# Kernel optimization log

Measured on AMD Instinct MI355X. Metric: run time of the kernel, lower is better.

## Reference

```python
import jax, jax.numpy as jnp
import numpy as np


def _reverse_padded(x, lengths):
    # x: [T, B, D]; reverse each sequence within its own length (packed-seq semantics)
    T = x.shape[0]
    t = jnp.arange(T)[:, None]                                   # [T, 1]
    idx = jnp.where(t < lengths[None, :], lengths[None, :] - 1 - t, t)  # [T, B]
    return jnp.take_along_axis(x, idx[:, :, None], axis=0)


def _lstm_dir(x, w_ih, w_hh, b):
    # single-direction LSTM, torch gate order (i, f, g, o). x: [T, B, Din]
    T, B, _ = x.shape
    H = w_hh.shape[1]
    xg = jnp.einsum('tbi,gi->tbg', x, w_ih) + b  # precompute input projections [T,B,4H]

    def step(carry, g_x):
        h, c = carry
        g = g_x + h @ w_hh.T
        i, f, gc, o = jnp.split(g, 4, axis=-1)
        c = jax.nn.sigmoid(f) * c + jax.nn.sigmoid(i) * jnp.tanh(gc)
        h = jax.nn.sigmoid(o) * jnp.tanh(c)
        return (h, c), h

    h0 = jnp.zeros((B, H), x.dtype)
    _, hs = jax.lax.scan(step, (h0, h0), xg)
    return hs  # [T, B, H]


def _bilstm_layer(x, lengths, wf, whf, bf, wr, whr, br):
    fwd = _lstm_dir(x, wf, whf, bf)
    rev = _reverse_padded(_lstm_dir(_reverse_padded(x, lengths), wr, whr, br), lengths)
    return jnp.concatenate([fwd, rev], axis=-1)  # [T, B, 2H]


def setup_inputs() -> dict:
    T, B, D, H = 256, 128, 300, 256
    key = jax.random.key(0)
    ks = jax.random.split(key, 24)
    stdv = 1.0 / np.sqrt(H)

    def u(k, shape):
        return jax.random.uniform(k, shape, jnp.float32, -stdv, stdv)

    inp = {
        'x': jax.random.normal(ks[0], (T, B, D), jnp.float32),
        'lengths': jax.random.randint(ks[1], (B,), 1, T + 1),
        # layer 0 forward / reverse
        'w_ih_l0': u(ks[2], (4 * H, D)), 'w_hh_l0': u(ks[3], (4 * H, H)),
        'b_ih_l0': u(ks[4], (4 * H,)), 'b_hh_l0': u(ks[5], (4 * H,)),
        'w_ih_l0r': u(ks[6], (4 * H, D)), 'w_hh_l0r': u(ks[7], (4 * H, H)),
        'b_ih_l0r': u(ks[8], (4 * H,)), 'b_hh_l0r': u(ks[9], (4 * H,)),
        # layer 1 forward / reverse (input dim 2H)
        'w_ih_l1': u(ks[10], (4 * H, 2 * H)), 'w_hh_l1': u(ks[11], (4 * H, H)),
        'b_ih_l1': u(ks[12], (4 * H,)), 'b_hh_l1': u(ks[13], (4 * H,)),
        'w_ih_l1r': u(ks[14], (4 * H, 2 * H)), 'w_hh_l1r': u(ks[15], (4 * H, H)),
        'b_ih_l1r': u(ks[16], (4 * H,)), 'b_hh_l1r': u(ks[17], (4 * H,)),
        # attention MLP + context vector
        'mlp_w': u(ks[18], (2 * H, 2 * H)),
        'mlp_b': u(ks[19], (2 * H,)),
        'ctx': jax.random.normal(ks[20], (2 * H,), jnp.float32) * 0.1,
    }
    return inp


def reference(x, lengths, w_ih_l0, w_hh_l0, b_ih_l0, b_hh_l0,
              w_ih_l0r, w_hh_l0r, b_ih_l0r, b_hh_l0r,
              w_ih_l1, w_hh_l1, b_ih_l1, b_hh_l1,
              w_ih_l1r, w_hh_l1r, b_ih_l1r, b_hh_l1r,
              mlp_w, mlp_b, ctx):
    lengths = jnp.maximum(lengths, 1)
    h1 = _bilstm_layer(x, lengths, w_ih_l0, w_hh_l0, b_ih_l0 + b_hh_l0,
                       w_ih_l0r, w_hh_l0r, b_ih_l0r + b_hh_l0r)
    h2 = _bilstm_layer(h1, lengths, w_ih_l1, w_hh_l1, b_ih_l1 + b_hh_l1,
                       w_ih_l1r, w_hh_l1r, b_ih_l1r + b_hh_l1r)
    out = h2.transpose(1, 0, 2)                                  # [B, T, 2H]
    ann = jnp.tanh(jnp.einsum('btd,ed->bte', out, mlp_w) + mlp_b)  # [B, T, 2H]
    scores = ann @ ctx                                           # [B, T]
    T = out.shape[1]
    mask = jnp.arange(T)[None, :] < lengths[:, None]             # [B, T]
    w = jax.nn.softmax(jnp.where(mask, scores, -1e9), axis=1)    # masked softmax over time
    return jnp.einsum('bt,btd->bd', w, out)                      # [B, 2H]
```

## Files before the change

### kernel.cpp

```cpp
#include <hip/hip_runtime.h>


#define T_ 256
#define B_ 128
#define D_ 300
#define H_ 256
#define G4H 1024
#define H2 512
#define LDK 40
#define LDA 264
#define XGS 76
#define RSLOTS 4

typedef __attribute__((ext_vector_type(8))) short bf16x8;
typedef __attribute__((ext_vector_type(4))) short short4v;
typedef __attribute__((ext_vector_type(4))) float f32x4;

#define MFMA16(a, b, c) __builtin_amdgcn_mfma_f32_16x16x32_bf16(a, b, c, 0, 0, 0)
#define ATOM_ST(p, v) __hip_atomic_store((p), (v), __ATOMIC_RELAXED, __HIP_MEMORY_SCOPE_AGENT)
#define ATOM_LD(p) __hip_atomic_load((p), __ATOMIC_RELAXED, __HIP_MEMORY_SCOPE_AGENT)

__device__ __forceinline__ float sigf(float x) { return 1.f / (1.f + __expf(-x)); }
__device__ __forceinline__ float tanhfast(float x) { return 2.f / (1.f + __expf(-2.f * x)) - 1.f; }

__device__ __forceinline__ short hi_bf16(float x) {
  return (short)(__float_as_uint(x) >> 16);
}
__device__ __forceinline__ short lo_bf16(float x) {
  float lo = x - __uint_as_float(__float_as_uint(x) & 0xFFFF0000u);
  return (short)(__float_as_uint(lo) >> 16);
}

__device__ __forceinline__ void split_f4(const float4 v, short* hp, short* lp) {
  short4v h, l;
  h.x = hi_bf16(v.x); l.x = lo_bf16(v.x);
  h.y = hi_bf16(v.y); l.y = lo_bf16(v.y);
  h.z = hi_bf16(v.z); l.z = lo_bf16(v.z);
  h.w = hi_bf16(v.w); l.w = lo_bf16(v.w);
  *(short4v*)hp = h;
  *(short4v*)lp = l;
}

__device__ __forceinline__ void split8(const float4 v0, const float4 v1,
                                       bf16x8* hp, bf16x8* lp) {
  bf16x8 h, l;
  h[0] = hi_bf16(v0.x); l[0] = lo_bf16(v0.x);
  h[1] = hi_bf16(v0.y); l[1] = lo_bf16(v0.y);
  h[2] = hi_bf16(v0.z); l[2] = lo_bf16(v0.z);
  h[3] = hi_bf16(v0.w); l[3] = lo_bf16(v0.w);
  h[4] = hi_bf16(v1.x); l[4] = lo_bf16(v1.x);
  h[5] = hi_bf16(v1.y); l[5] = lo_bf16(v1.y);
  h[6] = hi_bf16(v1.z); l[6] = lo_bf16(v1.z);
  h[7] = hi_bf16(v1.w); l[7] = lo_bf16(v1.w);
  *hp = h; *lp = l;
}

__global__ __launch_bounds__(256, 2) void proj_gemm2(
    const float* __restrict__ X,
    const float* __restrict__ W0, const float* __restrict__ W1,
    const float* __restrict__ b1f, const float* __restrict__ b2f,
    const float* __restrict__ b1r, const float* __restrict__ b2r,
// ... 136 lines not shown
      split_f4(wv, &Wh[ro], &Wl[ro]);
    }
    __syncthreads();

    bf16x8 ah[4], al[4], bh[4], bl[4];
#pragma unroll
    for (int mt = 0; mt < 4; mt++) {
      const int ro = (mb + mt * 16 + r16) * LDK + quad * 8;
      ah[mt] = *(const bf16x8*)&Xh[ro];
      al[mt] = *(const bf16x8*)&Xl[ro];
    }
#pragma unroll
    for (int nt = 0; nt < 4; nt++) {
      const int ro = (nb + nt * 16 + r16) * LDK + quad * 8;
      bh[nt] = *(const bf16x8*)&Wh[ro];
      bl[nt] = *(const bf16x8*)&Wl[ro];
    }
#pragma unroll
    for (int mt = 0; mt < 4; mt++)
#pragma unroll
      for (int nt = 0; nt < 4; nt++) {
        acc[mt][nt] = __builtin_amdgcn_mfma_f32_16x16x32_bf16(ah[mt], bh[nt], acc[mt][nt], 0, 0, 0);
        acc[mt][nt] = __builtin_amdgcn_mfma_f32_16x16x32_bf16(ah[mt], bl[nt], acc[mt][nt], 0, 0, 0);
        acc[mt][nt] = __builtin_amdgcn_mfma_f32_16x16x32_bf16(al[mt], bh[nt], acc[mt][nt], 0, 0, 0);
      }
    __syncthreads();
  }

  float bb4[4], cc4[4];
#pragma unroll
  for (int nt = 0; nt < 4; nt++) {
    const int col = n0 + nb + nt * 16 + r16;
    bb4[nt] = mlp_b[col];
    cc4[nt] = ctx[col];
  }
#pragma unroll
  for (int mt = 0; mt < 4; mt++) {
#pragma unroll
    for (int reg = 0; reg < 4; reg++) {
      float ssum = 0.f;
#pragma unroll
      for (int nt = 0; nt < 4; nt++)
        ssum += tanhfast(acc[mt][nt][reg] + bb4[nt]) * cc4[nt];
      ssum += __shfl_xor(ssum, 1);
      ssum += __shfl_xor(ssum, 2);
      ssum += __shfl_xor(ssum, 4);
      ssum += __shfl_xor(ssum, 8);
      if (r16 == 0)
        atomicAdd(&scores[m0 + mb + mt * 16 + quad * 4 + reg], ssum);
    }
  }
}

__global__ __launch_bounds__(256, 1) void lstm_fused(
    float* __restrict__ xgF, float* __restrict__ xgR,
    const float* __restrict__ XSRC,
    const float* __restrict__ whF, const float* __restrict__ whR,
    const float* __restrict__ wihF, const float* __restrict__ wihR,
    const float* __restrict__ b1f, const float* __restrict__ b2f,
    const float* __restrict__ b1r, const float* __restrict__ b2r,
    const int* __restrict__ lengths, float* __restrict__ hout,
    float* __restrict__ ring, int K)
{
  __shared__ short Ah[16 * LDA], Al[16 * LDA];
  __shared__ float gbuf[8 * 128];
  __shared__ short PXh[128 * LDK], PXl[128 * LDK];
  __shared__ short PWh[128 * LDK], PWl[128 * LDK];

  const int tid = threadIdx.x;
  const int blk = blockIdx.x;
  const int s = blk >> 5;
  const int d = (blk >> 4) & 1;
  const int g = blk & 15;
  float* __restrict__ xgd = d ? xgR : xgF;
  const float* __restrict__ wh = d ? whR : whF;
  const float* __restrict__ wih = d ? wihR : wihF;
  const float* __restrict__ bias1 = d ? b1r : b1f;
  const float* __restrict__ bias2 = d ? b2r : b2f;
  unsigned* __restrict__ ring32 = (unsigned*)ring;

  const int lane = tid & 63;
  const int w = tid >> 6;
  const int r16 = lane & 15, quad = lane >> 4;

  const int cb = tid >> 5;
  const int hl = tid & 31;
  const int b = g * 8 + cb;
  const int hdim = s * 32 + hl;
  const int k0 = hl * 8;

  const int sr = tid >> 3;
  const int sc = (tid & 7) * 4;
  const int mb = (w & 1) * 64, nb = (w >> 1) * 64;
  const int n0 = s * 128;
  const int KITERS = (K + 31) >> 5;

  bf16x8 bh[2][8], bl[2][8];
#pragma unroll
  for (int nt = 0; nt < 2; nt++)
#pragma unroll
    for (int kt = 0; kt < 8; kt++) {
      const float* wr = wh + (size_t)(w * 256 + s * 32 + nt * 16 + r16) * 256
                           + kt * 32 + quad * 8;
      float4 v0 = *(const float4*)(wr);
      float4 v1 = *(const float4*)(wr + 4);
      split8(v0, v1, &bh[nt][kt], &bl[nt][kt]);
    }

  f32x4 pacc[4][4];
#pragma unroll
  for (int i = 0; i < 4; i++)
#pragma unroll
    for (int j = 0; j < 4; j++) pacc[i][j] = (f32x4){0.f, 0.f, 0.f, 0.f};

  {
    int* za = (int*)Ah;
    int* zb = (int*)Al;
    for (int i = tid; i < (16 * LDA) / 2; i += 256) { za[i] = 0; zb[i] = 0; }
  }
  float c = 0.f;
  int lb = lengths[b]; if (lb < 1) lb = 1;
  const float* xr0 = xgd + (size_t)b * 1024 + hdim;
  float x0 = ATOM_LD(xr0), x1 = ATOM_LD(xr0 + 256);
  float x2 = ATOM_LD(xr0 + 512), x3 = ATOM_LD(xr0 + 768);
  __syncthreads();

  for (int t = 0; t < T_; t++) {
    const bool last = (t == T_ - 1);

    f32x4 aH0 = {0.f,0.f,0.f,0.f}, aM0 = {0.f,0.f,0.f,0.f}, aL0 = {0.f,0.f,0.f,0.f};
    f32x4 aH1 = {0.f,0.f,0.f,0.f}, aM1 = {0.f,0.f,0.f,0.f}, aL1 = {0.f,0.f,0.f,0.f};
#pragma unroll
    for (int kt = 0; kt < 8; kt++) {
      const int ro = r16 * LDA + kt * 32 + quad * 8;
      bf16x8 ahf = *(const bf16x8*)&Ah[ro];
      bf16x8 alf = *(const bf16x8*)&Al[ro];
      aH0 = MFMA16(ahf, bh[0][kt], aH0);
      aM0 = MFMA16(ahf, bl[0][kt], aM0);
      aL0 = MFMA16(alf, bh[0][kt], aL0);
      aH1 = MFMA16(ahf, bh[1][kt], aH1);
      aM1 = MFMA16(ahf, bl[1][kt], aM1);
      aL1 = MFMA16(alf, bh[1][kt], aL1);
    }
    if (quad < 2) {
#pragma unroll
      for (int reg = 0; reg < 4; reg++) {
        gbuf[(quad * 4 + reg) * 128 + w * 32 + r16]      = aH0[reg] + aM0[reg] + aL0[reg];
        gbuf[(quad * 4 + reg) * 128 + w * 32 + 16 + r16] = aH1[reg] + aM1[reg] + aL1[reg];
      }
    }
    __syncthreads();

    const float gi = gbuf[cb * 128 +       hl] + x0;
    const float gf = gbuf[cb * 128 +  32 + hl] + x1;
    const float gg = gbuf[cb * 128 +  64 + hl] + x2;
    const float go = gbuf[cb * 128 +  96 + hl] + x3;
    const float si = sigf(gi), sf = sigf(gf);
    const float tg = tanhfast(gg), so = sigf(go);
    c = sf * c + si * tg;
    const float h = so * tanhfast(c);
    if (!last) {
      const unsigned hu = (unsigned)(unsigned short)hi_bf16(h);
      const unsigned lu = (unsigned)(unsigned short)lo_bf16(h);
      const unsigned pv = (hu << 16) | (lu & 0xFFFEu) | (unsigned)((t >> 2) & 1);
      ATOM_ST(&ring32[(((t & 3) * 2 + d) * 128 + b) * 256 + hdim], pv);
    }
    const int tin = d ? ((t < lb) ? (lb - 1 - t) : t) : t;
    hout[((size_t)tin * 128 + b) * 512 + d * 256 + hdim] = h;

    if (t < 192) {
      const int wj = t >> 4, ki = t & 15;
      const int y = 64 + wj * 16 + g;
      if (ki < KITERS) {
        const int gk = ki * 32 + sc;
        const bool kin = (gk < K);
#pragma unroll
        for (int p = 0; p < 4; p++) {
          const int r = sr + p * 32;
          float4 xv = {0.f, 0.f, 0.f, 0.f}, wv = {0.f, 0.f, 0.f, 0.f};
          if (kin) {
            int ss = y;
            if (d) {
              int lbr = lengths[r]; if (lbr < 1) lbr = 1;
              ss = (y < lbr) ? (lbr - 1 - y) : y;
            }
            xv = *(const float4*)(XSRC + ((size_t)ss * 128 + r) * K + gk);
            wv = *(const float4*)(wih + (size_t)(n0 + r) * K + gk);
          }
          const int ro = (sr + p * 32) * LDK + sc;
          split_f4(xv, &PXh[ro], &PXl[ro]);
          split_f4(wv, &PWh[ro], &PWl[ro]);
        }
        __syncthreads();

        bf16x8 pah[4], pal[4], pbh[4], pbl[4];
#pragma unroll
        for (int mt = 0; mt < 4; mt++) {
          const int ro = (mb + mt * 16 + r16) * LDK + quad * 8;
          pah[mt] = *(const bf16x8*)&PXh[ro];
          pal[mt] = *(const bf16x8*)&PXl[ro];
        }
#pragma unroll
        for (int nt = 0; nt < 4; nt++) {
          const int ro = (nb + nt * 16 + r16) * LDK + quad * 8;
          pbh[nt] = *(const bf16x8*)&PWh[ro];
          pbl[nt] = *(const bf16x8*)&PWl[ro];
        }
#pragma unroll
        for (int mt = 0; mt < 4; mt++)
#pragma unroll
          for (int nt = 0; nt < 4; nt++) {
            pacc[mt][nt] = MFMA16(pah[mt], pbh[nt], pacc[mt][nt]);
            pacc[mt][nt] = MFMA16(pah[mt], pbl[nt], pacc[mt][nt]);
            pacc[mt][nt] = MFMA16(pal[mt], pbh[nt], pacc[mt][nt]);
          }
      }
      if (ki == 15) {
        const int yslot = y % XGS;
        float bsum[4];
#pragma unroll
        for (int nt = 0; nt < 4; nt++) {
          const int col = n0 + nb + nt * 16 + r16;
          bsum[nt] = bias1[col] + bias2[col];
        }
#pragma unroll
        for (int mt = 0; mt < 4; mt++) {
          const int row = mb + mt * 16 + quad * 4;
#pragma unroll
          for (int nt = 0; nt < 4; nt++) {
            const int col = n0 + nb + nt * 16 + r16;
            float* Cp = xgd + ((size_t)yslot * 128 + row) * 1024 + col;
#pragma unroll
            for (int reg = 0; reg < 4; reg++)
              ATOM_ST(&Cp[(size_t)reg * 1024], pacc[mt][nt][reg] + bsum[nt]);
            pacc[mt][nt] = (f32x4){0.f, 0.f, 0.f, 0.f};
          }
        }
      }
    }

    if (!last) {
      const int ns = (t + 1) % XGS;
      const float* xn = xgd + ((size_t)ns * 128 + b) * 1024 + hdim;
      const float nx0 = ATOM_LD(xn), nx1 = ATOM_LD(xn + 256);
      const float nx2 = ATOM_LD(xn + 512), nx3 = ATOM_LD(xn + 768);

      const unsigned* ru = ring32 + (((t & 3) * 2 + d) * 128 + g * 8 + cb) * 256 + k0;
      const unsigned par = (unsigned)((t >> 2) & 1);
      unsigned uv[8];
      int it = 0;
      for (;;) {
        bool ok = true;
#pragma unroll
        for (int j = 0; j < 8; j++) {
          uv[j] = ATOM_LD(&ru[j]);
          ok &= ((uv[j] & 1u) == par);
        }
        if (ok || ++it >= 100000) break;
      }
      bf16x8 hv, lv;
#pragma unroll
      for (int j = 0; j < 8; j++) {
        hv[j] = (short)(uv[j] >> 16);
        lv[j] = (short)(uv[j] & 0xFFFFu);
      }
      *(bf16x8*)&Ah[cb * LDA + k0] = hv;
      *(bf16x8*)&Al[cb * LDA + k0] = lv;

      x0 = nx0; x1 = nx1; x2 = nx2; x3 = nx3;
      __syncthreads();
    }
  }
}

__global__ __launch_bounds__(256) void attn_final(
    const float* __restrict__ h2, const float* __restrict__ scores,
    const int* __restrict__ lengths, float* __restrict__ out)
{
  __shared__ float sl[256];
  __shared__ float red[256];
  const int b = blockIdx.x, tid = threadIdx.x;
  int lb = lengths[b]; if (lb < 1) lb = 1;
  const float sc = scores[(size_t)tid * 128 + b];
  const bool valid = (tid < lb);
  red[tid] = valid ? sc : -1e30f;
  __syncthreads();
  for (int off = 128; off > 0; off >>= 1) {
    if (tid < off) red[tid] = fmaxf(red[tid], red[tid + off]);
    __syncthreads();
  }
  const float mx = red[0];
  __syncthreads();
  const float p = valid ? __expf(sc - mx) : 0.f;
  red[tid] = p;
  __syncthreads();
  for (int off = 128; off > 0; off >>= 1) {
    if (tid < off) red[tid] += red[tid + off];
    __syncthreads();
  }
  const float inv = 1.f / red[0];
  __syncthreads();
  sl[tid] = p * inv;
  __syncthreads();

  float ax = 0.f, ay = 0.f;
  const int dd = tid * 2;
  for (int t = 0; t < 256; t++) {
    const float w = sl[t];
    if (w != 0.f) {
      const float* row = h2 + ((size_t)t * 128 + b) * 512 + dd;
      ax += w * row[0];
      ay += w * row[1];
    }
  }
  float2 r; r.x = ax; r.y = ay;
  *(float2*)(out + (size_t)b * 512 + dd) = r;
}

extern "C" void kernel_launch(void* const* d_in, const int* in_sizes, int n_in,
                              void* d_out, int out_size, void* d_ws, size_t ws_size,
                              hipStream_t stream) {
  (void)in_sizes; (void)n_in; (void)out_size; (void)ws_size;
  const float* x        = (const float*)d_in[0];
  const int*   lengths  = (const int*)d_in[1];
  const float* w_ih_l0  = (const float*)d_in[2];
  const float* w_hh_l0  = (const float*)d_in[3];
  const float* b_ih_l0  = (const float*)d_in[4];
  const float* b_hh_l0  = (const float*)d_in[5];
  const float* w_ih_l0r = (const float*)d_in[6];
  const float* w_hh_l0r = (const float*)d_in[7];
  const float* b_ih_l0r = (const float*)d_in[8];
  const float* b_hh_l0r = (const float*)d_in[9];
  const float* w_ih_l1  = (const float*)d_in[10];
  const float* w_hh_l1  = (const float*)d_in[11];
  const float* b_ih_l1  = (const float*)d_in[12];
  const float* b_hh_l1  = (const float*)d_in[13];
  const float* w_ih_l1r = (const float*)d_in[14];
  const float* w_hh_l1r = (const float*)d_in[15];
  const float* b_ih_l1r = (const float*)d_in[16];
  const float* b_hh_l1r = (const float*)d_in[17];
  const float* mlp_w    = (const float*)d_in[18];
  const float* mlp_b    = (const float*)d_in[19];
  const float* ctx      = (const float*)d_in[20];
  float* out = (float*)d_out;

  float* ws = (float*)d_ws;
  const size_t XG76  = (size_t)XGS * B_ * G4H;
  const size_t H_SZ  = (size_t)T_ * B_ * H2;
  const size_t RINGF = (size_t)RSLOTS * 2 * B_ * H_;
  float* xgF    = ws;
  float* xgR    = xgF + XG76;
  float* h1     = xgR + XG76;
  float* h2     = h1 + H_SZ;
  float* ring   = h2 + H_SZ;
  float* scores = ring + RINGF;

  (void)hipMemsetAsync(scores, 0, 32768 * 4, stream);

  dim3 blk(256);
  const dim3 pgrid(G4H / 128, 64, 2);

  proj_gemm2<<<pgrid, blk, 0, stream>>>(x, w_ih_l0, w_ih_l0r,
                                        b_ih_l0, b_hh_l0, b_ih_l0r, b_hh_l0r,
                                        xgF, xgR, G4H, D_, lengths, 0);
  (void)hipMemsetAsync(ring, 0xFF, RINGF * 4, stream);
  lstm_fused<<<256, blk, 0, stream>>>(xgF, xgR, x, w_hh_l0, w_hh_l0r,
                                      w_ih_l0, w_ih_l0r,
                                      b_ih_l0, b_hh_l0, b_ih_l0r, b_hh_l0r,
                                      lengths, h1, ring, D_);
  proj_gemm2<<<pgrid, blk, 0, stream>>>(h1, w_ih_l1, w_ih_l1r,
                                        b_ih_l1, b_hh_l1, b_ih_l1r, b_hh_l1r,
                                        xgF, xgR, G4H, H2, lengths, 0);
  (void)hipMemsetAsync(ring, 0xFF, RINGF * 4, stream);
  lstm_fused<<<256, blk, 0, stream>>>(xgF, xgR, h1, w_hh_l1, w_hh_l1r,
                                      w_ih_l1, w_ih_l1r,
                                      b_ih_l1, b_hh_l1, b_ih_l1r, b_hh_l1r,
                                      lengths, h2, ring, H2);
  attn_gemm<<<dim3(H2 / 128, (T_ * B_) / 128), blk, 0, stream>>>(h2, mlp_w, mlp_b, ctx, scores, T_ * B_, H2, H2);
  attn_final<<<B_, blk, 0, stream>>>(h2, scores, lengths, out);
}
```

Before: 2.639 ms.

## Warp-specialize LSTM kernel: separate recurrence and projection waves with register prefetch

```diff
diff --git a/kernel.cpp b/kernel.cpp
--- a/kernel.cpp
+++ b/kernel.cpp
@@ -249,7 +249,7 @@
   }
 }
 
-__global__ __launch_bounds__(256, 1) void lstm_fused(
+__global__ __launch_bounds__(512, 2) void lstm_fused(
     float* __restrict__ xgF, float* __restrict__ xgR,
     const float* __restrict__ XSRC,
     const float* __restrict__ whF, const float* __restrict__ whR,
@@ -269,204 +269,247 @@
   const int s = blk >> 5;
   const int d = (blk >> 4) & 1;
   const int g = blk & 15;
+  const bool is_lstm = (tid < 256);
   float* __restrict__ xgd = d ? xgR : xgF;
   const float* __restrict__ wh = d ? whR : whF;
   const float* __restrict__ wih = d ? wihR : wihF;
   const float* __restrict__ bias1 = d ? b1r : b1f;
   const float* __restrict__ bias2 = d ? b2r : b2f;
   unsigned* __restrict__ ring32 = (unsigned*)ring;
-
+  const int KITERS = (K + 31) >> 5;
+
+  const int w = tid >> 6;
   const int lane = tid & 63;
-  const int w = tid >> 6;
   const int r16 = lane & 15, quad = lane >> 4;
-
-  const int cb = tid >> 5;
+  const int cb = (tid >> 5) & 7;
   const int hl = tid & 31;
   const int b = g * 8 + cb;
   const int hdim = s * 32 + hl;
   const int k0 = hl * 8;
 
-  const int sr = tid >> 3;
-  const int sc = (tid & 7) * 4;
-  const int mb = (w & 1) * 64, nb = (w >> 1) * 64;
+  const int pt = tid & 255;
+  const int sr = pt >> 3;
+  const int sc = (pt & 7) * 4;
+  const int w2 = pt >> 6;
+  const int pmb = (w2 & 1) * 64, pnb = (w2 >> 1) * 64;
+  const int pr16 = (pt & 63) & 15, pquad = (pt & 63) >> 4;
   const int n0 = s * 128;
-  const int KITERS = (K + 31) >> 5;
-
-  bf16x8 bh[2][8], bl[2][8];
-#pragma unroll
-  for (int nt = 0; nt < 2; nt++)
-#pragma unroll
-    for (int kt = 0; kt < 8; kt++) {
-      const float* wr = wh + (size_t)(w * 256 + s * 32 + nt * 16 + r16) * 256
-                           + kt * 32 + quad * 8;
-      float4 v0 = *(const float4*)(wr);
-      float4 v1 = *(const float4*)(wr + 4);
-      split8(v0, v1, &bh[nt][kt], &bl[nt][kt]);
-    }
-
-  f32x4 pacc[4][4];
-#pragma unroll
-  for (int i = 0; i < 4; i++)
-#pragma unroll
-    for (int j = 0; j < 4; j++) pacc[i][j] = (f32x4){0.f, 0.f, 0.f, 0.f};
 
   {
     int* za = (int*)Ah;
     int* zb = (int*)Al;
-    for (int i = tid; i < (16 * LDA) / 2; i += 256) { za[i] = 0; zb[i] = 0; }
-  }
+    for (int i = tid; i < (16 * LDA) / 2; i += 512) { za[i] = 0; zb[i] = 0; }
+  }
+
+  bf16x8 bh[2][8], bl[2][8];
   float c = 0.f;
-  int lb = lengths[b]; if (lb < 1) lb = 1;
-  const float* xr0 = xgd + (size_t)b * 1024 + hdim;
-  float x0 = ATOM_LD(xr0), x1 = ATOM_LD(xr0 + 256);
-  float x2 = ATOM_LD(xr0 + 512), x3 = ATOM_LD(xr0 + 768);
+  int lb = 1;
+  float x0 = 0.f, x1 = 0.f, x2 = 0.f, x3 = 0.f;
+  int lenp[4];
+  float4 pfX[4], pfW[4];
+  f32x4 pacc[4][4];
+
+  if (is_lstm) {
+#pragma unroll
+    for (int nt = 0; nt < 2; nt++)
+#pragma unroll
+      for (int kt = 0; kt < 8; kt++) {
+        const float* wr = wh + (size_t)(w * 256 + s * 32 + nt * 16 + r16) * 256
+                             + kt * 32 + quad * 8;
+        float4 v0 = *(const float4*)(wr);
+        float4 v1 = *(const float4*)(wr + 4);
+        split8(v0, v1, &bh[nt][kt], &bl[nt][kt]);
+      }
+    lb = lengths[b]; if (lb < 1) lb = 1;
+    const float* xr0 = xgd + (size_t)b * 1024 + hdim;
+    x0 = ATOM_LD(xr0); x1 = ATOM_LD(xr0 + 256);
+    x2 = ATOM_LD(xr0 + 512); x3 = ATOM_LD(xr0 + 768);
+  } else {
+#pragma unroll
+    for (int p = 0; p < 4; p++) {
+      int lv = lengths[sr + p * 32]; if (lv < 1) lv = 1;
+      lenp[p] = lv;
+    }
+#pragma unroll
+    for (int i = 0; i < 4; i++)
+#pragma unroll
+      for (int j = 0; j < 4; j++) pacc[i][j] = (f32x4){0.f, 0.f, 0.f, 0.f};
+    {
+      const int y = 64 + g;
+      const int gk = sc;
+#pragma unroll
+      for (int p = 0; p < 4; p++) {
+        const int r = sr + p * 32;
+        int ss = y;
+        if (d) ss = (y < lenp[p]) ? (lenp[p] - 1 - y) : y;
+        pfX[p] = *(const float4*)(XSRC + ((size_t)ss * 128 + r) * K + gk);
+        pfW[p] = *(const float4*)(wih + (size_t)(n0 + r) * K + gk);
+      }
+    }
+  }
   __syncthreads();
 
   for (int t = 0; t < T_; t++) {
     const bool last = (t == T_ - 1);
 
-    f32x4 aH0 = {0.f,0.f,0.f,0.f}, aM0 = {0.f,0.f,0.f,0.f}, aL0 = {0.f,0.f,0.f,0.f};
-    f32x4 aH1 = {0.f,0.f,0.f,0.f}, aM1 = {0.f,0.f,0.f,0.f}, aL1 = {0.f,0.f,0.f,0.f};
-#pragma unroll
-    for (int kt = 0; kt < 8; kt++) {
-      const int ro = r16 * LDA + kt * 32 + quad * 8;
-      bf16x8 ahf = *(const bf16x8*)&Ah[ro];
-      bf16x8 alf = *(const bf16x8*)&Al[ro];
-      aH0 = MFMA16(ahf, bh[0][kt], aH0);
-      aM0 = MFMA16(ahf, bl[0][kt], aM0);
-      aL0 = MFMA16(alf, bh[0][kt], aL0);
-      aH1 = MFMA16(ahf, bh[1][kt], aH1);
-      aM1 = MFMA16(ahf, bl[1][kt], aM1);
-      aL1 = MFMA16(alf, bh[1][kt], aL1);
-    }
-    if (quad < 2) {
-#pragma unroll
-      for (int reg = 0; reg < 4; reg++) {
-        gbuf[(quad * 4 + reg) * 128 + w * 32 + r16]      = aH0[reg] + aM0[reg] + aL0[reg];
-        gbuf[(quad * 4 + reg) * 128 + w * 32 + 16 + r16] = aH1[reg] + aM1[reg] + aL1[reg];
-      }
-    }
-    __syncthreads();
-
-    const float gi = gbuf[cb * 128 +       hl] + x0;
-    const float gf = gbuf[cb * 128 +  32 + hl] + x1;
-    const float gg = gbuf[cb * 128 +  64 + hl] + x2;
-    const float go = gbuf[cb * 128 +  96 + hl] + x3;
-    const float si = sigf(gi), sf = sigf(gf);
-    const float tg = tanhfast(gg), so = sigf(go);
-    c = sf * c + si * tg;
-    const float h = so * tanhfast(c);
-    if (!last) {
-      const unsigned hu = (unsigned)(unsigned short)hi_bf16(h);
-      const unsigned lu = (unsigned)(unsigned short)lo_bf16(h);
-      const unsigned pv = (hu << 16) | (lu & 0xFFFEu) | (unsigned)((t >> 2) & 1);
-      ATOM_ST(&ring32[(((t & 3) * 2 + d) * 128 + b) * 256 + hdim], pv);
-    }
-    const int tin = d ? ((t < lb) ? (lb - 1 - t) : t) : t;
-    hout[((size_t)tin * 128 + b) * 512 + d * 256 + hdim] = h;
-
-    if (t < 192) {
-      const int wj = t >> 4, ki = t & 15;
-      const int y = 64 + wj * 16 + g;
-      if (ki < KITERS) {
-        const int gk = ki * 32 + sc;
-        const bool kin = (gk < K);
-#pragma unroll
-        for (int p = 0; p < 4; p++) {
-          const int r = sr + p * 32;
-          float4 xv = {0.f, 0.f, 0.f, 0.f}, wv = {0.f, 0.f, 0.f, 0.f};
-          if (kin) {
-            int ss = y;
-            if (d) {
-              int lbr = lengths[r]; if (lbr < 1) lbr = 1;
-              ss = (y < lbr) ? (lbr - 1 - y) : y;
-            }
-            xv = *(const float4*)(XSRC + ((size_t)ss * 128 + r) * K + gk);
-            wv = *(const float4*)(wih + (size_t)(n0 + r) * K + gk);
-          }
-          const int ro = (sr + p * 32) * LDK + sc;
-          split_f4(xv, &PXh[ro], &PXl[ro]);
-          split_f4(wv, &PWh[ro], &PWl[ro]);
+    if (is_lstm) {
+      f32x4 aH0 = {0.f,0.f,0.f,0.f}, aM0 = {0.f,0.f,0.f,0.f}, aL0 = {0.f,0.f,0.f,0.f};
+      f32x4 aH1 = {0.f,0.f,0.f,0.f}, aM1 = {0.f,0.f,0.f,0.f}, aL1 = {0.f,0.f,0.f,0.f};
+#pragma unroll
+      for (int kt = 0; kt < 8; kt++) {
+        const int ro = r16 * LDA + kt * 32 + quad * 8;
+        bf16x8 ahf = *(const bf16x8*)&Ah[ro];
+        bf16x8 alf = *(const bf16x8*)&Al[ro];
+        aH0 = MFMA16(ahf, bh[0][kt], aH0);
+        aM0 = MFMA16(ahf, bl[0][kt], aM0);
+        aL0 = MFMA16(alf, bh[0][kt], aL0);
+        aH1 = MFMA16(ahf, bh[1][kt], aH1);
+        aM1 = MFMA16(ahf, bl[1][kt], aM1);
+        aL1 = MFMA16(alf, bh[1][kt], aL1);
+      }
+      if (quad < 2) {
+#pragma unroll
+        for (int reg = 0; reg < 4; reg++) {
+          gbuf[(quad * 4 + reg) * 128 + w * 32 + r16]      = aH0[reg] + aM0[reg] + aL0[reg];
+          gbuf[(quad * 4 + reg) * 128 + w * 32 + 16 + r16] = aH1[reg] + aM1[reg] + aL1[reg];
         }
-        __syncthreads();
-
-        bf16x8 pah[4], pal[4], pbh[4], pbl[4];
-#pragma unroll
-        for (int mt = 0; mt < 4; mt++) {
-          const int ro = (mb + mt * 16 + r16) * LDK + quad * 8;
-          pah[mt] = *(const bf16x8*)&PXh[ro];
-          pal[mt] = *(const bf16x8*)&PXl[ro];
-        }
-#pragma unroll
-        for (int nt = 0; nt < 4; nt++) {
-          const int ro = (nb + nt * 16 + r16) * LDK + quad * 8;
-          pbh[nt] = *(const bf16x8*)&PWh[ro];
-          pbl[nt] = *(const bf16x8*)&PWl[ro];
-        }
-#pragma unroll
-        for (int mt = 0; mt < 4; mt++)
-#pragma unroll
-          for (int nt = 0; nt < 4; nt++) {
-            pacc[mt][nt] = MFMA16(pah[mt], pbh[nt], pacc[mt][nt]);
-            pacc[mt][nt] = MFMA16(pah[mt], pbl[nt], pacc[mt][nt]);
-            pacc[mt][nt] = MFMA16(pal[mt], pbh[nt], pacc[mt][nt]);
-          }
-      }
-      if (ki == 15) {
-        const int yslot = y % XGS;
-        float bsum[4];
-#pragma unroll
-        for (int nt = 0; nt < 4; nt++) {
-          const int col = n0 + nb + nt * 16 + r16;
-          bsum[nt] = bias1[col] + bias2[col];
-        }
-#pragma unroll
-        for (int mt = 0; mt < 4; mt++) {
-          const int row = mb + mt * 16 + quad * 4;
-#pragma unroll
-          for (int nt = 0; nt < 4; nt++) {
-            const int col = n0 + nb + nt * 16 + r16;
-            float* Cp = xgd + ((size_t)yslot * 128 + row) * 1024 + col;
-#pragma unroll
-            for (int reg = 0; reg < 4; reg++)
-              ATOM_ST(&Cp[(size_t)reg * 1024], pacc[mt][nt][reg] + bsum[nt]);
-            pacc[mt][nt] = (f32x4){0.f, 0.f, 0.f, 0.f};
+      }
+    } else {
+      if (t < 192) {
+        const int ki = t & 15;
+        if (ki < KITERS) {
+#pragma unroll
+          for (int p = 0; p < 4; p++) {
+            const int gk = ki * 32 + sc;
+            const int ro = (sr + p * 32) * LDK + sc;
+            float4 xv = {0.f,0.f,0.f,0.f}, wv = {0.f,0.f,0.f,0.f};
+            if (gk < K) { xv = pfX[p]; wv = pfW[p]; }
+            split_f4(xv, &PXh[ro], &PXl[ro]);
+            split_f4(wv, &PWh[ro], &PWl[ro]);
           }
         }
       }
     }
-
-    if (!last) {
-      const int ns = (t + 1) % XGS;
-      const float* xn = xgd + ((size_t)ns * 128 + b) * 1024 + hdim;
-      const float nx0 = ATOM_LD(xn), nx1 = ATOM_LD(xn + 256);
-      const float nx2 = ATOM_LD(xn + 512), nx3 = ATOM_LD(xn + 768);
-
-      const unsigned* ru = ring32 + (((t & 3) * 2 + d) * 128 + g * 8 + cb) * 256 + k0;
-      const unsigned par = (unsigned)((t >> 2) & 1);
-      unsigned uv[8];
-      int it = 0;
-      for (;;) {
-        bool ok = true;
+    __syncthreads();
+
+    if (is_lstm) {
+      const float gi = gbuf[cb * 128 +       hl] + x0;
+      const float gf = gbuf[cb * 128 +  32 + hl] + x1;
+      const float gg = gbuf[cb * 128 +  64 + hl] + x2;
+      const float go = gbuf[cb * 128 +  96 + hl] + x3;
+      const float si = sigf(gi), sf = sigf(gf);
+      const float tg = tanhfast(gg), so = sigf(go);
+      c = sf * c + si * tg;
+      const float h = so * tanhfast(c);
+      if (!last) {
+        const unsigned hu = (unsigned)(unsigned short)hi_bf16(h);
+        const unsigned lu = (unsigned)(unsigned short)lo_bf16(h);
+        const unsigned pv = (hu << 16) | (lu & 0xFFFEu) | (unsigned)((t >> 2) & 1);
+        ATOM_ST(&ring32[(((t & 3) * 2 + d) * 128 + b) * 256 + hdim], pv);
+      }
+      const int tin = d ? ((t < lb) ? (lb - 1 - t) : t) : t;
+      hout[((size_t)tin * 128 + b) * 512 + d * 256 + hdim] = h;
+
+      if (!last) {
+        const int ns = (t + 1) % XGS;
+        const float* xn = xgd + ((size_t)ns * 128 + b) * 1024 + hdim;
+        const float nx0 = ATOM_LD(xn), nx1 = ATOM_LD(xn + 256);
+        const float nx2 = ATOM_LD(xn + 512), nx3 = ATOM_LD(xn + 768);
+
+        const unsigned* ru = ring32 + (((t & 3) * 2 + d) * 128 + g * 8 + cb) * 256 + k0;
+        const unsigned par = (unsigned)((t >> 2) & 1);
+        unsigned uv[8];
+        int it = 0;
+        for (;;) {
+          bool ok = true;
+#pragma unroll
+          for (int j = 0; j < 8; j++) {
+            uv[j] = ATOM_LD(&ru[j]);
+            ok &= ((uv[j] & 1u) == par);
+          }
+          if (ok || ++it >= 100000) break;
+        }
+        bf16x8 hv, lv;
 #pragma unroll
         for (int j = 0; j < 8; j++) {
-          uv[j] = ATOM_LD(&ru[j]);
-          ok &= ((uv[j] & 1u) == par);
+          hv[j] = (short)(uv[j] >> 16);
+          lv[j] = (short)(uv[j] & 0xFFFFu);
         }
-        if (ok || ++it >= 100000) break;
-      }
-      bf16x8 hv, lv;
-#pragma unroll
-      for (int j = 0; j < 8; j++) {
-        hv[j] = (short)(uv[j] >> 16);
-        lv[j] = (short)(uv[j] & 0xFFFFu);
-      }
-      *(bf16x8*)&Ah[cb * LDA + k0] = hv;
-      *(bf16x8*)&Al[cb * LDA + k0] = lv;
-
-      x0 = nx0; x1 = nx1; x2 = nx2; x3 = nx3;
-      __syncthreads();
-    }
+        *(bf16x8*)&Ah[cb * LDA + k0] = hv;
+        *(bf16x8*)&Al[cb * LDA + k0] = lv;
+
+        x0 = nx0; x1 = nx1; x2 = nx2; x3 = nx3;
+      }
+    } else {
+      if (t < 192) {
+        const int ki = t & 15;
+        if (ki < KITERS) {
+          bf16x8 pah[4], pal[4], pbh[4], pbl[4];
+#pragma unroll
+          for (int mt = 0; mt < 4; mt++) {
+            const int ro = (pmb + mt * 16 + pr16) * LDK + pquad * 8;
+            pah[mt] = *(const bf16x8*)&PXh[ro];
+            pal[mt] = *(const bf16x8*)&PXl[ro];
+          }
+#pragma unroll
+          for (int nt = 0; nt < 4; nt++) {
+            const int ro = (pnb + nt * 16 + pr16) * LDK + pquad * 8;
+            pbh[nt] = *(const bf16x8*)&PWh[ro];
+            pbl[nt] = *(const bf16x8*)&PWl[ro];
+          }
+#pragma unroll
+          for (int mt = 0; mt < 4; mt++)
+#pragma unroll
+            for (int nt = 0; nt < 4; nt++) {
+              pacc[mt][nt] = MFMA16(pah[mt], pbh[nt], pacc[mt][nt]);
+              pacc[mt][nt] = MFMA16(pah[mt], pbl[nt], pacc[mt][nt]);
+              pacc[mt][nt] = MFMA16(pal[mt], pbh[nt], pacc[mt][nt]);
+            }
+        }
+        if (ki == 15) {
+          const int y = 64 + (t >> 4) * 16 + g;
+          const int yslot = y % XGS;
+          float bsum[4];
+#pragma unroll
+          for (int nt = 0; nt < 4; nt++) {
+            const int col = n0 + pnb + nt * 16 + pr16;
+            bsum[nt] = bias1[col] + bias2[col];
+          }
+#pragma unroll
+          for (int mt = 0; mt < 4; mt++) {
+            const int row = pmb + mt * 16 + pquad * 4;
+#pragma unroll
+            for (int nt = 0; nt < 4; nt++) {
+              const int col = n0 + pnb + nt * 16 + pr16;
+              float* Cp = xgd + ((size_t)yslot * 128 + row) * 1024 + col;
+#pragma unroll
+              for (int reg = 0; reg < 4; reg++)
+                ATOM_ST(&Cp[(size_t)reg * 1024], pacc[mt][nt][reg] + bsum[nt]);
+              pacc[mt][nt] = (f32x4){0.f, 0.f, 0.f, 0.f};
+            }
+          }
+        }
+      }
+      const int tn = t + 1;
+      if (tn < 192) {
+        const int kin = tn & 15;
+        if (kin < KITERS) {
+          const int y = 64 + (tn >> 4) * 16 + g;
+          const int gk = kin * 32 + sc;
+          if (gk < K) {
+#pragma unroll
+            for (int p = 0; p < 4; p++) {
+              const int r = sr + p * 32;
+              int ss = y;
+              if (d) ss = (y < lenp[p]) ? (lenp[p] - 1 - y) : y;
+              pfX[p] = *(const float4*)(XSRC + ((size_t)ss * 128 + r) * K + gk);
+              pfW[p] = *(const float4*)(wih + (size_t)(n0 + r) * K + gk);
+            }
+          }
+        }
+      }
+    }
+    __syncthreads();
   }
 }
 
@@ -561,18 +604,18 @@
                                         b_ih_l0, b_hh_l0, b_ih_l0r, b_hh_l0r,
                                         xgF, xgR, G4H, D_, lengths, 0);
   (void)hipMemsetAsync(ring, 0xFF, RINGF * 4, stream);
-  lstm_fused<<<256, blk, 0, stream>>>(xgF, xgR, x, w_hh_l0, w_hh_l0r,
-                                      w_ih_l0, w_ih_l0r,
-                                      b_ih_l0, b_hh_l0, b_ih_l0r, b_hh_l0r,
-                                      lengths, h1, ring, D_);
+  lstm_fused<<<256, dim3(512), 0, stream>>>(xgF, xgR, x, w_hh_l0, w_hh_l0r,
+                                            w_ih_l0, w_ih_l0r,
+                                            b_ih_l0, b_hh_l0, b_ih_l0r, b_hh_l0r,
+                                            lengths, h1, ring, D_);
   proj_gemm2<<<pgrid, blk, 0, stream>>>(h1, w_ih_l1, w_ih_l1r,
                                         b_ih_l1, b_hh_l1, b_ih_l1r, b_hh_l1r,
                                         xgF, xgR, G4H, H2, lengths, 0);
   (void)hipMemsetAsync(ring, 0xFF, RINGF * 4, stream);
-  lstm_fused<<<256, blk, 0, stream>>>(xgF, xgR, h1, w_hh_l1, w_hh_l1r,
-                                      w_ih_l1, w_ih_l1r,
-                                      b_ih_l1, b_hh_l1, b_ih_l1r, b_hh_l1r,
-                                      lengths, h2, ring, H2);
+  lstm_fused<<<256, dim3(512), 0, stream>>>(xgF, xgR, h1, w_hh_l1, w_hh_l1r,
+                                            w_ih_l1, w_ih_l1r,
+                                            b_ih_l1, b_hh_l1, b_ih_l1r, b_hh_l1r,
+                                            lengths, h2, ring, H2);
   attn_gemm<<<dim3(H2 / 128, (T_ * B_) / 128), blk, 0, stream>>>(h2, mlp_w, mlp_b, ctx, scores, T_ * B_, H2, H2);
   attn_final<<<B_, blk, 0, stream>>>(h2, scores, lengths, out);
 }
```

Result: slower. 3.782 ms (+43.3%).

## Split LSTM recurrence into time chunks with separate projection blocks

Applied to the files above, without the earlier changes.

```diff
diff --git a/kernel.cpp b/kernel.cpp
--- a/kernel.cpp
+++ b/kernel.cpp
@@ -7,6 +7,7 @@
 #define H_ 256
 #define G4H 1024
 #define H2 512
+#define TC 64
 #define LDK 40
 #define LDA 264
 #define XGS 76
@@ -249,7 +250,7 @@
   }
 }
 
-__global__ __launch_bounds__(256, 1) void lstm_fused(
+__global__ __launch_bounds__(256, 2) void lstm_fused(
     float* __restrict__ xgF, float* __restrict__ xgR,
     const float* __restrict__ XSRC,
     const float* __restrict__ whF, const float* __restrict__ whR,
@@ -257,193 +258,64 @@
     const float* __restrict__ b1f, const float* __restrict__ b2f,
     const float* __restrict__ b1r, const float* __restrict__ b2r,
     const int* __restrict__ lengths, float* __restrict__ hout,
-    float* __restrict__ ring, int K)
+    float* __restrict__ ring, float* __restrict__ cbuf,
+    int* __restrict__ prog, int t0, int K, int do_proj)
 {
   __shared__ short Ah[16 * LDA], Al[16 * LDA];
   __shared__ float gbuf[8 * 128];
   __shared__ short PXh[128 * LDK], PXl[128 * LDK];
   __shared__ short PWh[128 * LDK], PWl[128 * LDK];
+  __shared__ int gflag;
 
   const int tid = threadIdx.x;
-  const int blk = blockIdx.x;
-  const int s = blk >> 5;
-  const int d = (blk >> 4) & 1;
-  const int g = blk & 15;
-  float* __restrict__ xgd = d ? xgR : xgF;
-  const float* __restrict__ wh = d ? whR : whF;
-  const float* __restrict__ wih = d ? wihR : wihF;
-  const float* __restrict__ bias1 = d ? b1r : b1f;
-  const float* __restrict__ bias2 = d ? b2r : b2f;
   unsigned* __restrict__ ring32 = (unsigned*)ring;
 
-  const int lane = tid & 63;
-  const int w = tid >> 6;
-  const int r16 = lane & 15, quad = lane >> 4;
-
-  const int cb = tid >> 5;
-  const int hl = tid & 31;
-  const int b = g * 8 + cb;
-  const int hdim = s * 32 + hl;
-  const int k0 = hl * 8;
-
-  const int sr = tid >> 3;
-  const int sc = (tid & 7) * 4;
-  const int mb = (w & 1) * 64, nb = (w >> 1) * 64;
-  const int n0 = s * 128;
-  const int KITERS = (K + 31) >> 5;
-
-  bf16x8 bh[2][8], bl[2][8];
-#pragma unroll
-  for (int nt = 0; nt < 2; nt++)
-#pragma unroll
-    for (int kt = 0; kt < 8; kt++) {
-      const float* wr = wh + (size_t)(w * 256 + s * 32 + nt * 16 + r16) * 256
-                           + kt * 32 + quad * 8;
-      float4 v0 = *(const float4*)(wr);
-      float4 v1 = *(const float4*)(wr + 4);
-      split8(v0, v1, &bh[nt][kt], &bl[nt][kt]);
-    }
-
-  f32x4 pacc[4][4];
-#pragma unroll
-  for (int i = 0; i < 4; i++)
-#pragma unroll
-    for (int j = 0; j < 4; j++) pacc[i][j] = (f32x4){0.f, 0.f, 0.f, 0.f};
-
-  {
-    int* za = (int*)Ah;
-    int* zb = (int*)Al;
-    for (int i = tid; i < (16 * LDA) / 2; i += 256) { za[i] = 0; zb[i] = 0; }
-  }
-  float c = 0.f;
-  int lb = lengths[b]; if (lb < 1) lb = 1;
-  const float* xr0 = xgd + (size_t)b * 1024 + hdim;
-  float x0 = ATOM_LD(xr0), x1 = ATOM_LD(xr0 + 256);
-  float x2 = ATOM_LD(xr0 + 512), x3 = ATOM_LD(xr0 + 768);
-  __syncthreads();
-
-  for (int t = 0; t < T_; t++) {
-    const bool last = (t == T_ - 1);
-
-    f32x4 aH0 = {0.f,0.f,0.f,0.f}, aM0 = {0.f,0.f,0.f,0.f}, aL0 = {0.f,0.f,0.f,0.f};
-    f32x4 aH1 = {0.f,0.f,0.f,0.f}, aM1 = {0.f,0.f,0.f,0.f}, aL1 = {0.f,0.f,0.f,0.f};
-#pragma unroll
-    for (int kt = 0; kt < 8; kt++) {
-      const int ro = r16 * LDA + kt * 32 + quad * 8;
-      bf16x8 ahf = *(const bf16x8*)&Ah[ro];
-      bf16x8 alf = *(const bf16x8*)&Al[ro];
-      aH0 = MFMA16(ahf, bh[0][kt], aH0);
-      aM0 = MFMA16(ahf, bl[0][kt], aM0);
-      aL0 = MFMA16(alf, bh[0][kt], aL0);
-      aH1 = MFMA16(ahf, bh[1][kt], aH1);
-      aM1 = MFMA16(ahf, bl[1][kt], aM1);
-      aL1 = MFMA16(alf, bh[1][kt], aL1);
-    }
-    if (quad < 2) {
-#pragma unroll
-      for (int reg = 0; reg < 4; reg++) {
-        gbuf[(quad * 4 + reg) * 128 + w * 32 + r16]      = aH0[reg] + aM0[reg] + aL0[reg];
-        gbuf[(quad * 4 + reg) * 128 + w * 32 + 16 + r16] = aH1[reg] + aM1[reg] + aL1[reg];
-      }
-    }
-    __syncthreads();
-
-    const float gi = gbuf[cb * 128 +       hl] + x0;
-    const float gf = gbuf[cb * 128 +  32 + hl] + x1;
-    const float gg = gbuf[cb * 128 +  64 + hl] + x2;
-    const float go = gbuf[cb * 128 +  96 + hl] + x3;
-    const float si = sigf(gi), sf = sigf(gf);
-    const float tg = tanhfast(gg), so = sigf(go);
-    c = sf * c + si * tg;
-    const float h = so * tanhfast(c);
-    if (!last) {
-      const unsigned hu = (unsigned)(unsigned short)hi_bf16(h);
-      const unsigned lu = (unsigned)(unsigned short)lo_bf16(h);
-      const unsigned pv = (hu << 16) | (lu & 0xFFFEu) | (unsigned)((t >> 2) & 1);
-      ATOM_ST(&ring32[(((t & 3) * 2 + d) * 128 + b) * 256 + hdim], pv);
-    }
-    const int tin = d ? ((t < lb) ? (lb - 1 - t) : t) : t;
-    hout[((size_t)tin * 128 + b) * 512 + d * 256 + hdim] = h;
-
-    if (t < 192) {
-      const int wj = t >> 4, ki = t & 15;
-      const int y = 64 + wj * 16 + g;
-      if (ki < KITERS) {
-        const int gk = ki * 32 + sc;
-        const bool kin = (gk < K);
-#pragma unroll
-        for (int p = 0; p < 4; p++) {
-          const int r = sr + p * 32;
-          float4 xv = {0.f, 0.f, 0.f, 0.f}, wv = {0.f, 0.f, 0.f, 0.f};
-          if (kin) {
-            int ss = y;
-            if (d) {
-              int lbr = lengths[r]; if (lbr < 1) lbr = 1;
-              ss = (y < lbr) ? (lbr - 1 - y) : y;
-            }
-            xv = *(const float4*)(XSRC + ((size_t)ss * 128 + r) * K + gk);
-            wv = *(const float4*)(wih + (size_t)(n0 + r) * K + gk);
-          }
-          const int ro = (sr + p * 32) * LDK + sc;
-          split_f4(xv, &PXh[ro], &PXl[ro]);
-          split_f4(wv, &PWh[ro], &PWl[ro]);
-        }
-        __syncthreads();
-
-        bf16x8 pah[4], pal[4], pbh[4], pbl[4];
-#pragma unroll
-        for (int mt = 0; mt < 4; mt++) {
-          const int ro = (mb + mt * 16 + r16) * LDK + quad * 8;
-          pah[mt] = *(const bf16x8*)&PXh[ro];
-          pal[mt] = *(const bf16x8*)&PXl[ro];
-        }
-#pragma unroll
-        for (int nt = 0; nt < 4; nt++) {
-          const int ro = (nb + nt * 16 + r16) * LDK + quad * 8;
-          pbh[nt] = *(const bf16x8*)&PWh[ro];
-          pbl[nt] = *(const bf16x8*)&PWl[ro];
-        }
-#pragma unroll
-        for (int mt = 0; mt < 4; mt++)
-#pragma unroll
-          for (int nt = 0; nt < 4; nt++) {
-            pacc[mt][nt] = MFMA16(pah[mt], pbh[nt], pacc[mt][nt]);
-            pacc[mt][nt] = MFMA16(pah[mt], pbl[nt], pacc[mt][nt]);
-            pacc[mt][nt] = MFMA16(pal[mt], pbh[nt], pacc[mt][nt]);
-          }
-      }
-      if (ki == 15) {
-        const int yslot = y % XGS;
-        float bsum[4];
-#pragma unroll
-        for (int nt = 0; nt < 4; nt++) {
-          const int col = n0 + nb + nt * 16 + r16;
-          bsum[nt] = bias1[col] + bias2[col];
-        }
-#pragma unroll
-        for (int mt = 0; mt < 4; mt++) {
-          const int row = mb + mt * 16 + quad * 4;
-#pragma unroll
-          for (int nt = 0; nt < 4; nt++) {
-            const int col = n0 + nb + nt * 16 + r16;
-            float* Cp = xgd + ((size_t)yslot * 128 + row) * 1024 + col;
-#pragma unroll
-            for (int reg = 0; reg < 4; reg++)
-              ATOM_ST(&Cp[(size_t)reg * 1024], pacc[mt][nt][reg] + bsum[nt]);
-            pacc[mt][nt] = (f32x4){0.f, 0.f, 0.f, 0.f};
-          }
-        }
-      }
-    }
-
-    if (!last) {
-      const int ns = (t + 1) % XGS;
-      const float* xn = xgd + ((size_t)ns * 128 + b) * 1024 + hdim;
-      const float nx0 = ATOM_LD(xn), nx1 = ATOM_LD(xn + 256);
-      const float nx2 = ATOM_LD(xn + 512), nx3 = ATOM_LD(xn + 768);
-
-      const unsigned* ru = ring32 + (((t & 3) * 2 + d) * 128 + g * 8 + cb) * 256 + k0;
-      const unsigned par = (unsigned)((t >> 2) & 1);
+  if (blockIdx.x < 256) {
+    const int blk = blockIdx.x;
+    const int s = blk >> 5;
+    const int d = (blk >> 4) & 1;
+    const int g = blk & 15;
+    float* __restrict__ xgd = d ? xgR : xgF;
+    const float* __restrict__ wh = d ? whR : whF;
+
+    const int lane = tid & 63;
+    const int w = tid >> 6;
+    const int r16 = lane & 15, quad = lane >> 4;
+    const int cb = tid >> 5;
+    const int hl = tid & 31;
+    const int b = g * 8 + cb;
+    const int hdim = s * 32 + hl;
+    const int k0 = hl * 8;
+
+    bf16x8 bh[2][8], bl[2][8];
+#pragma unroll
+    for (int nt = 0; nt < 2; nt++)
+#pragma unroll
+      for (int kt = 0; kt < 8; kt++) {
+        const float* wr = wh + (size_t)(w * 256 + s * 32 + nt * 16 + r16) * 256
+                             + kt * 32 + quad * 8;
+        float4 v0 = *(const float4*)(wr);
+        float4 v1 = *(const float4*)(wr + 4);
+        split8(v0, v1, &bh[nt][kt], &bl[nt][kt]);
+      }
+
+    {
+      int* za = (int*)(Ah + 8 * LDA);
+      int* zb = (int*)(Al + 8 * LDA);
+      for (int i = tid; i < (8 * LDA) / 2; i += 256) { za[i] = 0; zb[i] = 0; }
+    }
+
+    float c;
+    if (t0 == 0) {
+      int* za = (int*)Ah;
+      int* zb = (int*)Al;
+      for (int i = tid; i < (8 * LDA) / 2; i += 256) { za[i] = 0; zb[i] = 0; }
+      c = 0.f;
+    } else {
+      c = cbuf[((size_t)d * 128 + b) * 256 + hdim];
+      const int pslot = (t0 - 1) & 3;
+      const unsigned par = (unsigned)(((t0 - 1) >> 2) & 1);
+      const unsigned* ru = ring32 + (((size_t)pslot * 2 + d) * 128 + g * 8 + cb) * 256 + k0;
       unsigned uv[8];
       int it = 0;
       for (;;) {
@@ -463,9 +335,214 @@
       }
       *(bf16x8*)&Ah[cb * LDA + k0] = hv;
       *(bf16x8*)&Al[cb * LDA + k0] = lv;
-
-      x0 = nx0; x1 = nx1; x2 = nx2; x3 = nx3;
+    }
+    int lb = lengths[b]; if (lb < 1) lb = 1;
+
+    {
+      const float* xr0 = xgd + ((size_t)(t0 % XGS) * 128 + b) * 1024 + hdim;
+    }
+    const float* xr0 = xgd + ((size_t)(t0 % XGS) * 128 + b) * 1024 + hdim;
+    float x0 = ATOM_LD(xr0), x1 = ATOM_LD(xr0 + 256);
+    float x2 = ATOM_LD(xr0 + 512), x3 = ATOM_LD(xr0 + 768);
+    __syncthreads();
+
+    const int tend = t0 + TC;
+    for (int t = t0; t < tend; t++) {
+      if (t > t0 && s == 0 && tid == 0) ATOM_ST(&prog[d * 16 + g], t - 1);
+      const bool chend = (t == tend - 1);
+
+      f32x4 aH0 = {0.f,0.f,0.f,0.f}, aM0 = {0.f,0.f,0.f,0.f}, aL0 = {0.f,0.f,0.f,0.f};
+      f32x4 aH1 = {0.f,0.f,0.f,0.f}, aM1 = {0.f,0.f,0.f,0.f}, aL1 = {0.f,0.f,0.f,0.f};
+#pragma unroll
+      for (int kt = 0; kt < 8; kt++) {
+        const int ro = r16 * LDA + kt * 32 + quad * 8;
+        bf16x8 ahf = *(const bf16x8*)&Ah[ro];
+        bf16x8 alf = *(const bf16x8*)&Al[ro];
+        aH0 = MFMA16(ahf, bh[0][kt], aH0);
+        aM0 = MFMA16(ahf, bl[0][kt], aM0);
+        aL0 = MFMA16(alf, bh[0][kt], aL0);
+        aH1 = MFMA16(ahf, bh[1][kt], aH1);
+        aM1 = MFMA16(ahf, bl[1][kt], aM1);
+        aL1 = MFMA16(alf, bh[1][kt], aL1);
+      }
+      if (quad < 2) {
+#pragma unroll
+        for (int reg = 0; reg < 4; reg++) {
+          gbuf[(quad * 4 + reg) * 128 + w * 32 + r16]      = aH0[reg] + aM0[reg] + aL0[reg];
+          gbuf[(quad * 4 + reg) * 128 + w * 32 + 16 + r16] = aH1[reg] + aM1[reg] + aL1[reg];
+        }
+      }
       __syncthreads();
+
+      const float gi = gbuf[cb * 128 +       hl] + x0;
+      const float gf = gbuf[cb * 128 +  32 + hl] + x1;
+      const float gg = gbuf[cb * 128 +  64 + hl] + x2;
+      const float go = gbuf[cb * 128 +  96 + hl] + x3;
+      const float si = sigf(gi), sf = sigf(gf);
+      const float tg = tanhfast(gg), so = sigf(go);
+      c = sf * c + si * tg;
+      const float h = so * tanhfast(c);
+      if (t != T_ - 1) {
+        const unsigned hu = (unsigned)(unsigned short)hi_bf16(h);
+        const unsigned lu = (unsigned)(unsigned short)lo_bf16(h);
+        const unsigned pv = (hu << 16) | (lu & 0xFFFEu) | (unsigned)((t >> 2) & 1);
+        ATOM_ST(&ring32[(((size_t)(t & 3) * 2 + d) * 128 + b) * 256 + hdim], pv);
+      }
+      const int tin = d ? ((t < lb) ? (lb - 1 - t) : t) : t;
+      hout[((size_t)tin * 128 + b) * 512 + d * 256 + hdim] = h;
+
+      if (!chend) {
+        const int ns = (t + 1) % XGS;
+        const float* xn = xgd + ((size_t)ns * 128 + b) * 1024 + hdim;
+        const float nx0 = ATOM_LD(xn), nx1 = ATOM_LD(xn + 256);
+        const float nx2 = ATOM_LD(xn + 512), nx3 = ATOM_LD(xn + 768);
+
+        const unsigned* ru = ring32 + (((size_t)(t & 3) * 2 + d) * 128 + g * 8 + cb) * 256 + k0;
+        const unsigned par = (unsigned)((t >> 2) & 1);
+        unsigned uv[8];
+        int it = 0;
+        for (;;) {
+          bool ok = true;
+#pragma unroll
+          for (int j = 0; j < 8; j++) {
+            uv[j] = ATOM_LD(&ru[j]);
+            ok &= ((uv[j] & 1u) == par);
+          }
+          if (ok || ++it >= 100000) break;
+        }
+        bf16x8 hv, lv;
+#pragma unroll
+        for (int j = 0; j < 8; j++) {
+          hv[j] = (short)(uv[j] >> 16);
+          lv[j] = (short)(uv[j] & 0xFFFFu);
+        }
+        *(bf16x8*)&Ah[cb * LDA + k0] = hv;
+        *(bf16x8*)&Al[cb * LDA + k0] = lv;
+
+        x0 = nx0; x1 = nx1; x2 = nx2; x3 = nx3;
+        __syncthreads();
+      }
+    }
+    cbuf[((size_t)d * 128 + b) * 256 + hdim] = c;
+
+  } else {
+    if (!do_proj) return;
+    const int p = blockIdx.x - 256;
+    const int sr = tid >> 3;
+    const int sc = (tid & 7) * 4;
+    const int lane = tid & 63, w2 = tid >> 6;
+    const int mb = (w2 & 1) * 64, nb = (w2 >> 1) * 64;
+    const int r16 = lane & 15, quad = lane >> 4;
+    const int KITERS = (K + 31) >> 5;
+
+    for (int jj = 0; jj < 4; jj++) {
+      const int J = p + 256 * jj;
+      const int nd = J & 15;
+      const int n0 = (nd >> 1) * 128;
+      const int dp = nd & 1;
+      const int yy = J >> 4;
+      const int y = t0 + 64 + yy;
+      float* __restrict__ xgd = dp ? xgR : xgF;
+      const float* __restrict__ wih = dp ? wihR : wihF;
+      const float* __restrict__ bias1 = dp ? b1r : b1f;
+      const float* __restrict__ bias2 = dp ? b2r : b2f;
+
+      const float* px[4];
+      const float* pw[4];
+#pragma unroll
+      for (int q = 0; q < 4; q++) {
+        const int r = sr + q * 32;
+        int ss = y;
+        if (dp) {
+          int lbr = lengths[r]; if (lbr < 1) lbr = 1;
+          ss = (y < lbr) ? (lbr - 1 - y) : y;
+        }
+        px[q] = XSRC + (size_t)(ss * 128 + r) * K;
+        pw[q] = wih + (size_t)(n0 + r) * K;
+      }
+
+      f32x4 acc[4][4];
+#pragma unroll
+      for (int i = 0; i < 4; i++)
+#pragma unroll
+        for (int j = 0; j < 4; j++) acc[i][j] = (f32x4){0.f, 0.f, 0.f, 0.f};
+
+      for (int ki = 0; ki < KITERS; ki++) {
+        const int gk = ki * 32 + sc;
+        const bool kin = (gk < K);
+#pragma unroll
+        for (int q = 0; q < 4; q++) {
+          float4 xv = {0.f, 0.f, 0.f, 0.f}, wv = {0.f, 0.f, 0.f, 0.f};
+          if (kin) { xv = *(const float4*)(px[q] + gk); wv = *(const float4*)(pw[q] + gk); }
+          const int ro = (sr + q * 32) * LDK + sc;
+          split_f4(xv, &PXh[ro], &PXl[ro]);
+          split_f4(wv, &PWh[ro], &PWl[ro]);
+        }
+        __syncthreads();
+
+        bf16x8 ah[4], al[4], wbh[4], wbl[4];
+#pragma unroll
+        for (int mt = 0; mt < 4; mt++) {
+          const int ro = (mb + mt * 16 + r16) * LDK + quad * 8;
+          ah[mt] = *(const bf16x8*)&PXh[ro];
+          al[mt] = *(const bf16x8*)&PXl[ro];
+        }
+#pragma unroll
+        for (int nt = 0; nt < 4; nt++) {
+          const int ro = (nb + nt * 16 + r16) * LDK + quad * 8;
+          wbh[nt] = *(const bf16x8*)&PWh[ro];
+          wbl[nt] = *(const bf16x8*)&PWl[ro];
+        }
+#pragma unroll
+        for (int mt = 0; mt < 4; mt++)
+#pragma unroll
+          for (int nt = 0; nt < 4; nt++) {
+            acc[mt][nt] = MFMA16(ah[mt], wbh[nt], acc[mt][nt]);
+            acc[mt][nt] = MFMA16(ah[mt], wbl[nt], acc[mt][nt]);
+            acc[mt][nt] = MFMA16(al[mt], wbh[nt], acc[mt][nt]);
+          }
+        __syncthreads();
+      }
+
+      {
+        const int need = y - 74;
+        int itg = 0;
+        for (;;) {
+          if (tid == 0) {
+            int m = 0x7fffffff;
+#pragma unroll
+            for (int i = 0; i < 16; i++) {
+              const int v = ATOM_LD(&prog[dp * 16 + i]);
+              m = (v < m) ? v : m;
+            }
+            gflag = (m >= need) ? 1 : 0;
+          }
+          __syncthreads();
+          const int ok = gflag;
+          __syncthreads();
+          if (ok || ++itg >= 300000) break;
+        }
+      }
+
+      const int yslot = y % XGS;
+      float bsum[4];
+#pragma unroll
+      for (int nt = 0; nt < 4; nt++) {
+        const int col = n0 + nb + nt * 16 + r16;
+        bsum[nt] = bias1[col] + bias2[col];
+      }
+#pragma unroll
+      for (int mt = 0; mt < 4; mt++) {
+        const int row = mb + mt * 16 + quad * 4;
+#pragma unroll
+        for (int nt = 0; nt < 4; nt++) {
+          const int col = n0 + nb + nt * 16 + r16;
+          float* Cp = xgd + ((size_t)yslot * 128 + row) * 1024 + col;
+#pragma unroll
+          for (int reg = 0; reg < 4; reg++)
+            ATOM_ST(&Cp[(size_t)reg * 1024], acc[mt][nt][reg] + bsum[nt]);
+        }
+      }
     }
   }
 }
@@ -542,15 +619,17 @@
   float* out = (float*)d_out;
 
   float* ws = (float*)d_ws;
-  const size_t XG76  = (size_t)XGS * B_ * G4H;
-  const size_t H_SZ  = (size_t)T_ * B_ * H2;
-  const size_t RINGF = (size_t)RSLOTS * 2 * B_ * H_;
+  const size_t XGRING = (size_t)XGS * B_ * G4H;
+  const size_t H_SZ   = (size_t)T_ * B_ * H2;
+  const size_t RINGF  = (size_t)RSLOTS * 2 * B_ * H_;
   float* xgF    = ws;
-  float* xgR    = xgF + XG76;
-  float* h1     = xgR + XG76;
+  float* xgR    = xgF + XGRING;
+  float* h1     = xgR + XGRING;
   float* h2     = h1 + H_SZ;
   float* ring   = h2 + H_SZ;
-  float* scores = ring + RINGF;
+  float* cbuf   = ring + RINGF;
+  float* scores = cbuf + 65536;
+  int*   prog   = (int*)(scores + 32768);
 
   (void)hipMemsetAsync(scores, 0, 32768 * 4, stream);
 
@@ -561,18 +640,26 @@
                                         b_ih_l0, b_hh_l0, b_ih_l0r, b_hh_l0r,
                                         xgF, xgR, G4H, D_, lengths, 0);
   (void)hipMemsetAsync(ring, 0xFF, RINGF * 4, stream);
-  lstm_fused<<<256, blk, 0, stream>>>(xgF, xgR, x, w_hh_l0, w_hh_l0r,
-                                      w_ih_l0, w_ih_l0r,
-                                      b_ih_l0, b_hh_l0, b_ih_l0r, b_hh_l0r,
-                                      lengths, h1, ring, D_);
+  (void)hipMemsetAsync(prog, 0xFF, 32 * 4, stream);
+  for (int c = 0; c < 4; c++) {
+    lstm_fused<<<512, blk, 0, stream>>>(xgF, xgR, x, w_hh_l0, w_hh_l0r,
+                                        w_ih_l0, w_ih_l0r,
+                                        b_ih_l0, b_hh_l0, b_ih_l0r, b_hh_l0r,
+                                        lengths, h1, ring, cbuf, prog,
+                                        c * TC, D_, (c < 3) ? 1 : 0);
+  }
   proj_gemm2<<<pgrid, blk, 0, stream>>>(h1, w_ih_l1, w_ih_l1r,
                                         b_ih_l1, b_hh_l1, b_ih_l1r, b_hh_l1r,
                                         xgF, xgR, G4H, H2, lengths, 0);
   (void)hipMemsetAsync(ring, 0xFF, RINGF * 4, stream);
-  lstm_fused<<<256, blk, 0, stream>>>(xgF, xgR, h1, w_hh_l1, w_hh_l1r,
-                                      w_ih_l1, w_ih_l1r,
-                                      b_ih_l1, b_hh_l1, b_ih_l1r, b_hh_l1r,
-                                      lengths, h2, ring, H2);
+  (void)hipMemsetAsync(prog, 0xFF, 32 * 4, stream);
+  for (int c = 0; c < 4; c++) {
+    lstm_fused<<<512, blk, 0, stream>>>(xgF, xgR, h1, w_hh_l1, w_hh_l1r,
+                                        w_ih_l1, w_ih_l1r,
+                                        b_ih_l1, b_hh_l1, b_ih_l1r, b_hh_l1r,
+                                        lengths, h2, ring, cbuf, prog,
+                                        c * TC, H2, (c < 3) ? 1 : 0);
+  }
   attn_gemm<<<dim3(H2 / 128, (T_ * B_) / 128), blk, 0, stream>>>(h2, mlp_w, mlp_b, ctx, scores, T_ * B_, H2, H2);
   attn_final<<<B_, blk, 0, stream>>>(h2, scores, lengths, out);
 }
```

Result: faster. 2.235 ms (-15.3%).
